# Performance work log

Hardware: AMD Instinct MI355X
Metric: run time of the kernel (lower is better)

## Reference

```python
import jax, jax.numpy as jnp
import numpy as np

B, T = 256, 64
A, H, E = 32, 512, 16


def setup_inputs() -> dict:
    key = jax.random.key(0)
    ks = jax.random.split(key, 6)
    return {
        "actions": jax.random.normal(ks[0], (B, T, A), jnp.float32),
        "timesteps": jax.random.uniform(ks[1], (B,), jnp.float32),
        "cat_ids": jax.random.randint(ks[2], (B,), 0, E),
        "W1": 0.02 * jax.random.normal(ks[3], (E, A, H), jnp.float32),
        "b1": jnp.zeros((E, H), jnp.float32),
        "W2": 0.02 * jax.random.normal(ks[4], (E, 2 * H, H), jnp.float32),
        "b2": jnp.zeros((E, H), jnp.float32),
        "W3": 0.02 * jax.random.normal(ks[5], (E, H, H), jnp.float32),
        "b3": jnp.zeros((E, H), jnp.float32),
    }


def _cat_linear(x, W, b, cat_ids):
    # per-sample gathered weight: W[cat_ids] -> (B, d_in, d_out); bmm + bias
    return jnp.einsum('btd,bdh->bth', x, W[cat_ids]) + b[cat_ids][:, None, :]


def _pos_encoding(t, dim):
    # t: (B, T) float timesteps -> (B, T, dim) sinusoidal encoding
    half = dim // 2
    freqs = jnp.exp(-jnp.arange(half, dtype=jnp.float32) * (np.log(10000.0) / (half - 1)))
    ang = t[..., None] * freqs  # (B, T, half)
    return jnp.concatenate([jnp.sin(ang), jnp.cos(ang)], axis=-1)


def reference(actions, timesteps, cat_ids, W1, b1, W2, b2, W3, b3):
    Bb, Tt, _ = actions.shape
    hidden = W1.shape[-1]
    ts = jnp.broadcast_to(timesteps[:, None], (Bb, Tt))  # replicate scalar t across T
    a_emb = _cat_linear(actions, W1, b1, cat_ids)          # (B, T, H)
    tau_emb = _pos_encoding(ts, hidden).astype(a_emb.dtype)  # (B, T, H)
    x = jnp.concatenate([a_emb, tau_emb], axis=-1)         # (B, T, 2H)
    h = _cat_linear(x, W2, b2, cat_ids)
    x = h * jax.nn.sigmoid(h)                               # swish
    return _cat_linear(x, W3, b3, cat_ids)                  # (B, T, H)
```

## Files before the change

kernel.cpp:

```cpp
#include <hip/hip_runtime.h>

typedef __attribute__((ext_vector_type(8))) short bf16x8;
typedef __attribute__((ext_vector_type(4))) float f32x4;

namespace {
constexpr int NB = 256, NT = 64, NA = 32, NH = 512, NE = 16;
constexpr int NK2 = 32;
constexpr int NK3 = 16;
constexpr int NK  = NK2 + NK3;
constexpr int LDAu = 520;

constexpr size_t W1P_OFF = 0;
constexpr size_t W1P_SZ  = (size_t)NE * 32 * 64 * 16;
constexpr size_t W2P_OFF = W1P_OFF + W1P_SZ;
constexpr size_t W2P_SZ  = (size_t)NE * NK2 * 32 * 64 * 16;
constexpr size_t W3P_OFF = W2P_OFF + W2P_SZ;
constexpr size_t W3P_SZ  = (size_t)NE * NK3 * 32 * 64 * 16;
constexpr size_t PERM_OFF = W3P_OFF + W3P_SZ;
constexpr size_t WS_NEED  = PERM_OFF + (size_t)NB * 4;
}

__device__ __forceinline__ unsigned f2bf(float x) {
    union { float f; unsigned u; } v; v.f = x;
    return (v.u + 0x7FFFu + ((v.u >> 16) & 1u)) >> 16;
}
__device__ __forceinline__ f32x4 MFMA(bf16x8 a, bf16x8 b, f32x4 c) {
    return __builtin_amdgcn_mfma_f32_16x16x32_bf16(a, b, c, 0, 0, 0);
}

__global__ void pack_weights(const float* __restrict__ W1,
                             const float* __restrict__ W2,
                             const float* __restrict__ W3,
                             const int*   __restrict__ cat_ids,
                             unsigned char* __restrict__ ws)
{
    const int idx = blockIdx.x * 256 + threadIdx.x;
    constexpr int NF2 = NE * NK2 * 32 * 64;
    constexpr int NF3 = NE * NK3 * 32 * 64;
    constexpr int NF1 = NE * 32 * 64;

    const float* src = nullptr;
    uint4* dst = nullptr;
    int fi = 0, kbase = 0;
    bool have = true;
    if (idx < NF2) {
        fi = idx;
        const int ks = (fi >> 11) & 31;
        kbase = (ks < 16) ? (512 + ks * 32) : ((ks - 16) * 32);
        src = W2 + (size_t)(fi >> 16) * 1024 * NH;
        dst = (uint4*)(ws + W2P_OFF);
    } else if (idx < NF2 + NF3) {
        fi = idx - NF2;
        kbase = ((fi >> 11) & 15) * 32;
        src = W3 + (size_t)(fi >> 15) * NH * NH;
        dst = (uint4*)(ws + W3P_OFF);
    } else if (idx < NF2 + NF3 + NF1) {
        fi = idx - NF2 - NF3;
        kbase = 0;
        src = W1 + (size_t)(fi >> 11) * NA * NH;
        dst = (uint4*)(ws + W1P_OFF);
    } else have = false;

    if (have) {
        const int lane = fi & 63;
        const int nt   = (fi >> 6) & 31;
        const int k0   = kbase + ((lane >> 4) << 3);
        const int n    = nt * 16 + (lane & 15);
        unsigned rr[4];
        #pragma unroll
        for (int p = 0; p < 4; ++p) {
            const unsigned lo = f2bf(src[(size_t)(k0 + 2*p    ) * NH + n]);
            const unsigned hi = f2bf(src[(size_t)(k0 + 2*p + 1) * NH + n]);
            rr[p] = lo | (hi << 16);
        }
        uint4 r; r.x = rr[0]; r.y = rr[1]; r.z = rr[2]; r.w = rr[3];
        dst[fi] = r;
    }

    if (blockIdx.x == 0) {
        __shared__ int cs[NB];
        const int bb = threadIdx.x;
        cs[bb] = cat_ids[bb];
        __syncthreads();
        const int my = cs[bb];
        int rank = 0;
        #pragma unroll 8
        for (int i = 0; i < NB; ++i) {
            const int c = cs[i];
            rank += (c < my) || (c == my && i < bb);
        }
        ((int*)(ws + PERM_OFF))[rank] = bb;
    }
}

__global__ __launch_bounds__(1024, 4)
void me_enc_mfma6(const float* __restrict__ actions,
                  const float* __restrict__ timesteps,
                  const int*   __restrict__ cat_ids,
                  const float* __restrict__ b1,
                  const float* __restrict__ b2,
                  const float* __restrict__ b3,
                  const unsigned char* __restrict__ ws,
                  float* __restrict__ out)
{
    __shared__ unsigned short A0[NT * LDAu];
    __shared__ unsigned short A1[NT * LDAu];
    __shared__ unsigned tau_u32[NH / 2];

    const int bid  = blockIdx.x;
    const int tid  = threadIdx.x;
    const int lane = tid & 63;
    const int wn   = tid >> 6;
    const int lr   = lane & 15;
    const int lg   = lane >> 4;
    const int col0 = wn * 32;

    const int sidx = ((bid & 7) << 5) | (bid >> 3);
    const int* __restrict__ perm = (const int*)(ws + PERM_OFF);
    const int b    = perm[sidx];
    const int cat  = cat_ids[b];
    const float t  = timesteps[b];

    const uint4* __restrict__ wp2 =
        (const uint4*)(ws + W2P_OFF) + (size_t)cat * NK2 * 2048 + (size_t)(2 * wn) * 64 + lane;
    const uint4* __restrict__ wp3 =
        (const uint4*)(ws + W3P_OFF) + (size_t)cat * NK3 * 2048 + (size_t)(2 * wn) * 64 + lane;

    uint4 buf0_0, buf0_1, buf1_0, buf1_1, buf2_0, buf2_1,
          buf3_0, buf3_1, buf4_0, buf4_1;

#define LOADB(S, kk)                                                            \
    if ((kk) < NK) {                                                            \
        const uint4* bp_ = ((kk) < NK2) ? (wp2 + (size_t)(kk) * 2048)           \
                                        : (wp3 + (size_t)((kk) - NK2) * 2048);  \
        buf##S##_0 = bp_[0];                                                    \
        buf##S##_1 = bp_[64];                                                   \
    }

    LOADB(0, 0) LOADB(1, 1) LOADB(2, 2)

    if (tid < 256) {
        const int i0 = (2 * tid) & 255, i1 = i0 + 1;
        const float f0 = __expf(-(float)i0 * 0.036118981f);
        const float f1 = __expf(-(float)i1 * 0.036118981f);
        float v0, v1;
        if (tid < 128) { v0 = __sinf(t * f0); v1 = __sinf(t * f1); }
        else           { v0 = __cosf(t * f0); v1 = __cosf(t * f1); }
        tau_u32[tid] = f2bf(v0) | (f2bf(v1) << 16);
    }

    float bias1[2], bias2[2], bias3[2];
    #pragma unroll
    for (int j = 0; j < 2; ++j) {
        const int c = cat * NH + col0 + j * 16 + lr;
        bias1[j] = b1[c]; bias2[j] = b2[c]; bias3[j] = b3[c];
    }
    const uint4* __restrict__ w1p =
        (const uint4*)(ws + W1P_OFF) + (size_t)cat * 2048 + (size_t)(2 * wn) * 64 + lane;
    const uint4 w1f0 = w1p[0];
    const uint4 w1f1 = w1p[64];

    bf16x8 aact[4];
    #pragma unroll
    for (int mt = 0; mt < 4; ++mt) {
        const float* ap = actions + ((size_t)b * NT + mt * 16 + lr) * NA + lg * 8;
        const float4 a0 = ((const float4*)ap)[0];
        const float4 a1 = ((const float4*)ap)[1];
        bf16x8 v;
        v[0] = (short)f2bf(a0.x); v[1] = (short)f2bf(a0.y);
        v[2] = (short)f2bf(a0.z); v[3] = (short)f2bf(a0.w);
        v[4] = (short)f2bf(a1.x); v[5] = (short)f2bf(a1.y);
        v[6] = (short)f2bf(a1.z); v[7] = (short)f2bf(a1.w);
        aact[mt] = v;
    }

    __syncthreads();

    f32x4 acc[4][2];

    #pragma unroll
    for (int j = 0; j < 2; ++j) {
        const f32x4 v = {bias1[j], bias1[j], bias1[j], bias1[j]};
        #pragma unroll
        for (int mt = 0; mt < 4; ++mt) acc[mt][j] = v;
    }
    {
        union { uint4 u; bf16x8 v; } w0_, w1_;
        w0_.u = w1f0; w1_.u = w1f1;
        #pragma unroll
        for (int mt = 0; mt < 4; ++mt) {
            acc[mt][0] = MFMA(aact[mt], w0_.v, acc[mt][0]);
            acc[mt][1] = MFMA(aact[mt], w1_.v, acc[mt][1]);
        }
    }
    #pragma unroll
    for (int mt = 0; mt < 4; ++mt)
        #pragma unroll
        for (int j = 0; j < 2; ++j)
            #pragma unroll
            for (int r = 0; r < 4; ++r)
                A0[(mt*16 + lg*4 + r) * LDAu + col0 + j*16 + lr] =
                    (unsigned short)f2bf(acc[mt][j][r]);

    LOADB(3, 3) LOADB(4, 4)

    #pragma unroll
    for (int j = 0; j < 2; ++j) {
        const f32x4 v = {bias2[j], bias2[j], bias2[j], bias2[j]};
        #pragma unroll
        for (int mt = 0; mt < 4; ++mt) acc[mt][j] = v;
    }

    const unsigned short* __restrict__ tau_us = (const unsigned short*)tau_u32;

#define STEPK(S, kk)                                                            \
    if ((kk) < NK) {                                                            \
        if ((kk) == 16) {                                                       \
            asm volatile("s_waitcnt lgkmcnt(0)" ::: "memory");                  \
            __builtin_amdgcn_sched_barrier(0);                                  \
            __builtin_amdgcn_s_barrier();                    \
            __builtin_amdgcn_sched_barrier(0);                                  \
        }                                                                       \
        if ((kk) == NK2) {                                                      \
            _Pragma("unroll")                                                   \
            for (int mt_ = 0; mt_ < 4; ++mt_)                                   \
                _Pragma("unroll")                                               \
                for (int j_ = 0; j_ < 2; ++j_)                                  \
                    _Pragma("unroll")                                           \
                    for (int r_ = 0; r_ < 4; ++r_) {                            \
                        const float h_  = acc[mt_][j_][r_];                     \
                        const float sw_ = h_ / (1.f + __expf(-h_));             \
                        A1[(mt_*16 + lg*4 + r_) * LDAu + col0 + j_*16 + lr] =   \
                            (unsigned short)f2bf(sw_);                          \
                    }                                                           \
            _Pragma("unroll")                                                   \
            for (int j_ = 0; j_ < 2; ++j_) {                                    \
                const f32x4 v_ = {bias3[j_], bias3[j_], bias3[j_], bias3[j_]};  \
                _Pragma("unroll")                                               \
                for (int mt_ = 0; mt_ < 4; ++mt_) acc[mt_][j_] = v_;            \
            }                                                                   \
            asm volatile("s_waitcnt lgkmcnt(0)" ::: "memory");                  \
            __builtin_amdgcn_sched_barrier(0);                                  \
            __builtin_amdgcn_s_barrier();                    \
            __builtin_amdgcn_sched_barrier(0);                                  \
        }                                                                       \
        bf16x8 af0, af1, af2, af3;                                              \
        if ((kk) < 16) {                                                        \
            af0 = *(const bf16x8*)&tau_us[(kk) * 32 + lg * 8];                  \
            af1 = af0; af2 = af0; af3 = af0;                                    \
        } else if ((kk) < NK2) {                                                \
            const int ko_ = ((kk) - 16) * 32 + lg * 8;                          \
            af0 = *(const bf16x8*)&A0[(lr     ) * LDAu + ko_];                  \
            af1 = *(const bf16x8*)&A0[(lr + 16) * LDAu + ko_];                  \
            af2 = *(const bf16x8*)&A0[(lr + 32) * LDAu + ko_];                  \
            af3 = *(const bf16x8*)&A0[(lr + 48) * LDAu + ko_];                  \
        } else {                                                                \
            const int ko_ = ((kk) - NK2) * 32 + lg * 8;                         \
            af0 = *(const bf16x8*)&A1[(lr     ) * LDAu + ko_];                  \
            af1 = *(const bf16x8*)&A1[(lr + 16) * LDAu + ko_];                  \
            af2 = *(const bf16x8*)&A1[(lr + 32) * LDAu + ko_];                  \
            af3 = *(const bf16x8*)&A1[(lr + 48) * LDAu + ko_];                  \
        }                                                                       \
        union { uint4 u; bf16x8 v; } w0_, w1_;                                  \
        w0_.u = buf##S##_0; w1_.u = buf##S##_1;                                 \
        acc[0][0] = MFMA(af0, w0_.v, acc[0][0]);                                \
        acc[1][0] = MFMA(af1, w0_.v, acc[1][0]);                                \
        acc[2][0] = MFMA(af2, w0_.v, acc[2][0]);                                \
        acc[3][0] = MFMA(af3, w0_.v, acc[3][0]);                                \
        acc[0][1] = MFMA(af0, w1_.v, acc[0][1]);                                \
        acc[1][1] = MFMA(af1, w1_.v, acc[1][1]);                                \
        acc[2][1] = MFMA(af2, w1_.v, acc[2][1]);                                \
        acc[3][1] = MFMA(af3, w1_.v, acc[3][1]);                                \
    }

#define GROUP5(K0)                                                              \
    STEPK(0, (K0) + 0) LOADB(0, (K0) + 5)                                       \
    STEPK(1, (K0) + 1) LOADB(1, (K0) + 6)                                       \
    STEPK(2, (K0) + 2) LOADB(2, (K0) + 7)                                       \
    STEPK(3, (K0) + 3) LOADB(3, (K0) + 8)                                       \
    STEPK(4, (K0) + 4) LOADB(4, (K0) + 9)

    GROUP5(0)  GROUP5(5)  GROUP5(10) GROUP5(15) GROUP5(20)
    GROUP5(25) GROUP5(30) GROUP5(35) GROUP5(40) GROUP5(45)

#undef GROUP5
#undef STEPK
#undef LOADB

    #pragma unroll
    for (int mt = 0; mt < 4; ++mt)
        #pragma unroll
        for (int j = 0; j < 2; ++j)
            #pragma unroll
            for (int r = 0; r < 4; ++r)
                out[((size_t)b * NT + mt*16 + lg*4 + r) * NH + col0 + j*16 + lr] =
                    acc[mt][j][r];
}

__global__ __launch_bounds__(512, 2)
void me_enc_fused(const float* __restrict__ actions,
                  const float* __restrict__ timesteps,
                  const int*   __restrict__ cat_ids,
                  const float* __restrict__ W1,
                  const float* __restrict__ b1,
                  const float* __restrict__ W2,
                  const float* __restrict__ b2,
                  const float* __restrict__ W3,
                  const float* __restrict__ b3,
                  float* __restrict__ out)
{
    __shared__ float tau_s[NH];
    __shared__ float tauc_s[NH];
    __shared__ float act_s[16 * NA];
    __shared__ float buf_s[16][NH];

    const int b   = blockIdx.x;
    const int tid = threadIdx.x;
    const int cat = cat_ids[b];
    const float t = timesteps[b];

    const float* __restrict__ W1c = W1 + (size_t)cat * NA * NH;
    const float* __restrict__ W2c = W2 + (size_t)cat * 2 * NH * NH;
    const float* __restrict__ W2t = W2c + (size_t)NH * NH;
    const float* __restrict__ W3c = W3 + (size_t)cat * NH * NH;

    {
        const int i = tid & 255;
        const float f   = __expf(-(float)i * 0.036118981f);
        const float ang = t * f;
        tau_s[tid] = (tid < 256) ? __sinf(ang) : __cosf(ang);
    }
    __syncthreads();
    {
        float c0 = 0.f;
        for (int k = 0; k < NH; ++k)
            c0 += tau_s[k] * W2t[(size_t)k * NH + tid];
        tauc_s[tid] = b2[cat * NH + tid] + c0;
    }
    const float b1v = b1[cat * NH + tid];
    const int j2  = tid & 255;
    const int tl0 = (tid >> 8) * 8;
    const float b3v0 = b3[cat * NH + j2];
    const float b3v1 = b3[cat * NH + j2 + 256];
    const size_t obase = (size_t)b * NT * NH;
    float acc0[8], acc1[8];

    for (int t0 = 0; t0 < NT; t0 += 16) {
        act_s[tid] = actions[(size_t)b*NT*NA + (size_t)(t0 + (tid >> 5))*NA + (tid & 31)];
        __syncthreads();
        {
            float a_[16];
            #pragma unroll
            for (int l = 0; l < 16; ++l) a_[l] = b1v;
            for (int a = 0; a < NA; ++a) {
                const float w = W1c[(size_t)a * NH + tid];
                #pragma unroll
                for (int l = 0; l < 16; ++l) a_[l] += act_s[l*NA + a] * w;
            }
            #pragma unroll
            for (int l = 0; l < 16; ++l) buf_s[l][tid] = a_[l];
        }
        __syncthreads();
        {
            const float tc0 = tauc_s[j2], tc1 = tauc_s[j2 + 256];
            #pragma unroll
            for (int l = 0; l < 8; ++l) { acc0[l] = tc0; acc1[l] = tc1; }
            for (int k = 0; k < NH; ++k) {
                const float wa = W2c[(size_t)k*NH + j2];
                const float wb = W2c[(size_t)k*NH + j2 + 256];
                #pragma unroll
                for (int l = 0; l < 8; ++l) {
                    const float av = buf_s[tl0 + l][k];
                    acc0[l] += av * wa; acc1[l] += av * wb;
                }
            }
        }
        __syncthreads();
        #pragma unroll
        for (int l = 0; l < 8; ++l) {
            buf_s[tl0 + l][j2]       = acc0[l] / (1.f + __expf(-acc0[l]));
            buf_s[tl0 + l][j2 + 256] = acc1[l] / (1.f + __expf(-acc1[l]));
        }
        __syncthreads();
        {
            #pragma unroll
            for (int l = 0; l < 8; ++l) { acc0[l] = b3v0; acc1[l] = b3v1; }
            for (int k = 0; k < NH; ++k) {
                const float wa = W3c[(size_t)k*NH + j2];
                const float wb = W3c[(size_t)k*NH + j2 + 256];
                #pragma unroll
                for (int l = 0; l < 8; ++l) {
                    const float av = buf_s[tl0 + l][k];
                    acc0[l] += av * wa; acc1[l] += av * wb;
                }
            }
            #pragma unroll
            for (int l = 0; l < 8; ++l) {
                out[obase + (size_t)(t0 + tl0 + l)*NH + j2]       = acc0[l];
                out[obase + (size_t)(t0 + tl0 + l)*NH + j2 + 256] = acc1[l];
            }
        }
        __syncthreads();
    }
}

extern "C" void kernel_launch(void* const* d_in, const int* in_sizes, int n_in,
                              void* d_out, int out_size, void* d_ws, size_t ws_size,
                              hipStream_t stream)
{
    const float* actions   = (const float*)d_in[0];
    const float* timesteps = (const float*)d_in[1];
    const int*   cat_ids   = (const int*)  d_in[2];
    const float* W1 = (const float*)d_in[3];
    const float* b1 = (const float*)d_in[4];
    const float* W2 = (const float*)d_in[5];
    const float* b2 = (const float*)d_in[6];
    const float* W3 = (const float*)d_in[7];
    const float* b3 = (const float*)d_in[8];
    float* out = (float*)d_out;

    (void)in_sizes; (void)n_in; (void)out_size;

    if (ws_size >= WS_NEED) {
        unsigned char* ws = (unsigned char*)d_ws;
        constexpr int PACK_THREADS = NE*NK2*32*64 + NE*NK3*32*64 + NE*32*64;
        pack_weights<<<(PACK_THREADS + 255)/256, 256, 0, stream>>>(W1, W2, W3, cat_ids, ws);
        me_enc_mfma6<<<NB, 1024, 0, stream>>>(actions, timesteps, cat_ids,
                                              b1, b2, b3, ws, out);
    } else {
        me_enc_fused<<<NB, 512, 0, stream>>>(actions, timesteps, cat_ids,
                                             W1, b1, W2, b2, W3, b3, out);
    }
}
```

Measured before the change: 48.89 us.

## Deepen weight prefetch to six stages with inline-asm loads and explicit vmcnt waits

Weight fragments for the fused layer-2/3 K loop are now fetched with inline-asm global_load_dwordx4 instructions into six rotating register buffers instead of five. Each step waits with a hand-set s_waitcnt vmcnt count so only the oldest load must have landed, rather than letting the compiler insert conservative waits. The prefetch is moved after the first barrier and the bias values are pinned in registers. The aim is to keep more global loads in flight and hide memory latency behind MFMA work. The cost is more VGPR pressure and fragile manual wait counts that depend on exactly how many loads are outstanding.

New measurement: 47.57 us. 1.03x faster.

```diff
diff --git a/kernel.cpp b/kernel.cpp
--- a/kernel.cpp
+++ b/kernel.cpp
@@ -94,7 +94,7 @@
 }
 
 __global__ __launch_bounds__(1024, 4)
-void me_enc_mfma6(const float* __restrict__ actions,
+void me_enc_mfma7(const float* __restrict__ actions,
                   const float* __restrict__ timesteps,
                   const int*   __restrict__ cat_ids,
                   const float* __restrict__ b1,
@@ -105,7 +105,7 @@
 {
     __shared__ unsigned short A0[NT * LDAu];
     __shared__ unsigned short A1[NT * LDAu];
-    __shared__ unsigned tau_u32[NH / 2];
+    __shared__ alignas(16) unsigned tau_u32[NH / 2];
 
     const int bid  = blockIdx.x;
     const int tid  = threadIdx.x;
@@ -125,19 +125,6 @@
         (const uint4*)(ws + W2P_OFF) + (size_t)cat * NK2 * 2048 + (size_t)(2 * wn) * 64 + lane;
     const uint4* __restrict__ wp3 =
         (const uint4*)(ws + W3P_OFF) + (size_t)cat * NK3 * 2048 + (size_t)(2 * wn) * 64 + lane;
-
-    uint4 buf0_0, buf0_1, buf1_0, buf1_1, buf2_0, buf2_1,
-          buf3_0, buf3_1, buf4_0, buf4_1;
-
-#define LOADB(S, kk)                                                            \
-    if ((kk) < NK) {                                                            \
-        const uint4* bp_ = ((kk) < NK2) ? (wp2 + (size_t)(kk) * 2048)           \
-                                        : (wp3 + (size_t)((kk) - NK2) * 2048);  \
-        buf##S##_0 = bp_[0];                                                    \
-        buf##S##_1 = bp_[64];                                                   \
-    }
-
-    LOADB(0, 0) LOADB(1, 1) LOADB(2, 2)
 
     if (tid < 256) {
         const int i0 = (2 * tid) & 255, i1 = i0 + 1;
@@ -174,7 +161,26 @@
         aact[mt] = v;
     }
 
+    asm volatile("" :: "v"(bias2[0]), "v"(bias2[1]),
+                       "v"(bias3[0]), "v"(bias3[1]));
+
     __syncthreads();
+
+    uint4 buf0_0, buf0_1, buf1_0, buf1_1, buf2_0, buf2_1,
+          buf3_0, buf3_1, buf4_0, buf4_1, buf5_0, buf5_1;
+
+#define LOADB(S, kk)                                                            \
+    if ((kk) < NK) {                                                            \
+        const char* bp_ = (const char*)(((kk) < NK2)                            \
+            ? (const void*)(wp2 + (size_t)(kk) * 2048)                          \
+            : (const void*)(wp3 + (size_t)((kk) - NK2) * 2048));                \
+        asm volatile("global_load_dwordx4 %0, %2, off\n\t"                      \
+                     "global_load_dwordx4 %1, %2, off offset:1024"              \
+                     : "=&v"(buf##S##_0), "=&v"(buf##S##_1)                     \
+                     : "v"(bp_));                                               \
+    }
+
+    LOADB(0, 0) LOADB(1, 1) LOADB(2, 2) LOADB(3, 3) LOADB(4, 4) LOADB(5, 5)
 
     f32x4 acc[4][2];
 
@@ -202,8 +208,6 @@
                 A0[(mt*16 + lg*4 + r) * LDAu + col0 + j*16 + lr] =
                     (unsigned short)f2bf(acc[mt][j][r]);
 
-    LOADB(3, 3) LOADB(4, 4)
-
     #pragma unroll
     for (int j = 0; j < 2; ++j) {
         const f32x4 v = {bias2[j], bias2[j], bias2[j], bias2[j]};
@@ -213,7 +217,7 @@
 
     const unsigned short* __restrict__ tau_us = (const unsigned short*)tau_u32;
 
-#define STEPK(S, kk)                                                            \
+#define STEPK(S, kk, VM)                                                        \
     if ((kk) < NK) {                                                            \
         if ((kk) == 16) {                                                       \
             asm volatile("s_waitcnt lgkmcnt(0)" ::: "memory");                  \
@@ -244,6 +248,8 @@
             __builtin_amdgcn_s_barrier();                    \
             __builtin_amdgcn_sched_barrier(0);                                  \
         }                                                                       \
+        asm volatile("s_waitcnt vmcnt(" #VM ")");                               \
+        __builtin_amdgcn_sched_barrier(0);                                      \
         bf16x8 af0, af1, af2, af3;                                              \
         if ((kk) < 16) {                                                        \
             af0 = *(const bf16x8*)&tau_us[(kk) * 32 + lg * 8];                  \
@@ -273,17 +279,24 @@
         acc[3][1] = MFMA(af3, w1_.v, acc[3][1]);                                \
     }
 
-#define GROUP5(K0)                                                              \
-    STEPK(0, (K0) + 0) LOADB(0, (K0) + 5)                                       \
-    STEPK(1, (K0) + 1) LOADB(1, (K0) + 6)                                       \
-    STEPK(2, (K0) + 2) LOADB(2, (K0) + 7)                                       \
-    STEPK(3, (K0) + 3) LOADB(3, (K0) + 8)                                       \
-    STEPK(4, (K0) + 4) LOADB(4, (K0) + 9)
-
-    GROUP5(0)  GROUP5(5)  GROUP5(10) GROUP5(15) GROUP5(20)
-    GROUP5(25) GROUP5(30) GROUP5(35) GROUP5(40) GROUP5(45)
-
-#undef GROUP5
+#define GROUP6(K0)                                                              \
+    STEPK(0, (K0) + 0, 10) LOADB(0, (K0) + 6)                                   \
+    STEPK(1, (K0) + 1, 10) LOADB(1, (K0) + 7)                                   \
+    STEPK(2, (K0) + 2, 10) LOADB(2, (K0) + 8)                                   \
+    STEPK(3, (K0) + 3, 10) LOADB(3, (K0) + 9)                                   \
+    STEPK(4, (K0) + 4, 10) LOADB(4, (K0) + 10)                                  \
+    STEPK(5, (K0) + 5, 10) LOADB(5, (K0) + 11)
+
+    GROUP6(0)  GROUP6(6)  GROUP6(12) GROUP6(18)
+    GROUP6(24) GROUP6(30) GROUP6(36)
+    STEPK(0, 42, 10)
+    STEPK(1, 43, 8)
+    STEPK(2, 44, 6)
+    STEPK(3, 45, 4)
+    STEPK(4, 46, 2)
+    STEPK(5, 47, 0)
+
+#undef GROUP6
 #undef STEPK
 #undef LOADB
 
@@ -425,7 +438,7 @@
         unsigned char* ws = (unsigned char*)d_ws;
         constexpr int PACK_THREADS = NE*NK2*32*64 + NE*NK3*32*64 + NE*32*64;
         pack_weights<<<(PACK_THREADS + 255)/256, 256, 0, stream>>>(W1, W2, W3, cat_ids, ws);
-        me_enc_mfma6<<<NB, 1024, 0, stream>>>(actions, timesteps, cat_ids,
+        me_enc_mfma7<<<NB, 1024, 0, stream>>>(actions, timesteps, cat_ids,
                                               b1, b2, b3, ws, out);
     } else {
         me_enc_fused<<<NB, 512, 0, stream>>>(actions, timesteps, cat_ids,
```
